# Kernel tuning notes

Hardware: AMD Instinct MI355X
Metric: run time of the kernel (lower is better)

Reference implementation:

```python
import jax, jax.numpy as jnp
import numpy as np

B, H, W = 32, 512, 384
V, F = 6890, 13776


def setup_inputs() -> dict:
    key = jax.random.key(0)
    ks = jax.random.split(key, 8)
    scale = jnp.array([W, H, 1.0], dtype=jnp.float32)
    verts_1 = jax.random.uniform(ks[0], (B, V, 3), dtype=jnp.float32) * scale
    verts_2 = jax.random.uniform(ks[1], (B, V, 3), dtype=jnp.float32) * scale
    # face index per pixel; -1 = background (uint32 0xFFFFFFFF sentinel in original)
    vis_1 = (jax.random.randint(ks[2], (B, H, W), 0, F + 1) - 1).astype(jnp.int32)
    vis_2 = (jax.random.randint(ks[3], (B, H, W), 0, F + 1) - 1).astype(jnp.int32)
    face = jax.random.randint(ks[4], (F, 3), 0, V).astype(jnp.int32)
    vis_sym_mask_1 = (jax.random.uniform(ks[5], (B, H, W)) < 0.5).astype(jnp.float32)
    sym = jax.random.randint(ks[6], (V,), 0, V)
    symmetric_table = jnp.concatenate([sym, jnp.array([-1])]).astype(jnp.int32)
    return {"verts_1": verts_1, "vis_1": vis_1, "verts_2": verts_2, "vis_2": vis_2,
            "face": face, "vis_sym_mask_1": vis_sym_mask_1, "symmetric_table": symmetric_table}


def _pix_grid(h, w):
    # (x, y) pixel coordinates, shape [h, w, 2]
    x = jnp.arange(w, dtype=jnp.float32)
    y = jnp.arange(h, dtype=jnp.float32)
    return jnp.stack(jnp.meshgrid(x, y, indexing="xy"), axis=-1)


def reference(verts_1, vis_1, verts_2, vis_2, face, vis_sym_mask_1, symmetric_table):
    v1 = verts_1[:, :, :2]  # [B,V,2]
    v2 = verts_2[:, :, :2]
    bg = vis_1 < 0
    fc = jnp.where(bg, 0, vis_1)  # safe face id per pixel

    # --- vis_2_onehot: which faces are visible in image 2 ---
    valid2 = vis_2 >= 0
    idx2 = jnp.where(valid2, vis_2, 0)
    bidx = jnp.arange(B)[:, None, None]
    vf2 = jnp.zeros((B, F), jnp.int32).at[bidx, idx2].add(valid2.astype(jnp.int32)) > 0

    # --- cal_corr: barycentric correspondence per pixel ---
    tri = face[fc]  # [B,H,W,3] vertex ids of the face under each pixel
    gather = jax.vmap(lambda verts, t: verts[t])  # per-batch fancy gather
    p1 = gather(v1, tri)  # [B,H,W,3,2] face verts in img1
    p = _pix_grid(H, W)  # [H,W,2]
    a, b_, c = p1[..., 0, :], p1[..., 1, :], p1[..., 2, :]
    e0, e1, e2 = b_ - a, c - a, p - a
    d00 = (e0 * e0).sum(-1); d01 = (e0 * e1).sum(-1); d11 = (e1 * e1).sum(-1)
    d20 = (e2 * e0).sum(-1); d21 = (e2 * e1).sum(-1)
    denom = d00 * d11 - d01 * d01
    denom = jnp.where(jnp.abs(denom) < 1e-12, 1.0, denom)
    wv = (d11 * d20 - d01 * d21) / denom
    ww = (d00 * d21 - d01 * d20) / denom
    bary = jnp.stack([1.0 - wv - ww, wv, ww], axis=-1)  # [B,H,W,3]

    vis2f = vf2[bidx, fc]  # face visible in img2?
    sym_tri = symmetric_table[tri]  # symmetric vertex ids (-1 = none)
    sym_ok = jnp.all(sym_tri >= 0, axis=-1) & (vis_sym_mask_1 > 0)
    use_sym = (~vis2f) & sym_ok & (~bg)
    tri2 = jnp.where(use_sym[..., None], jnp.where(sym_tri >= 0, sym_tri, 0), tri)
    p2 = gather(v2, tri2)  # [B,H,W,3,2] face verts in img2
    corr = jnp.einsum("bhwk,bhwkc->bhwc", bary, p2)  # [B,H,W,2] (u,v)

    has_corr = (~bg) & (vis2f | use_sym)
    corr_mask = jnp.where(bg, 2.0, jnp.where(has_corr, 0.0, 1.0)).astype(jnp.float32)
    corr = jnp.where(has_corr[..., None], corr, 0.0)

    # custom kernel outputs are detached in the original
    corr = jax.lax.stop_gradient(corr)
    corr_mask = jax.lax.stop_gradient(corr_mask)

    # --- pad to square ---
    pad = (H - W) // 2
    corr = corr + jnp.array([pad, 0], dtype=corr.dtype)
    corr = jnp.pad(corr, ((0, 0), (0, 0), (pad, pad), (0, 0)))
    corr_mask = jnp.pad(corr_mask[..., None], ((0, 0), (0, 0), (pad, pad), (0, 0)),
                        constant_values=2.0)  # [B,H,W+2p,1]
    Hp, Wp = H, W + 2 * pad

    # --- corr_to_flow (HWC) then fix_flow: grid = base + (corr - base), normalized ---
    base = _pix_grid(Hp, Wp)  # [Hp,Wp,2]
    flow = corr - base
    grid = base + flow
    gx = 2.0 * grid[..., 0] / max(Wp - 1, 1) - 1.0
    gy = 2.0 * grid[..., 1] / max(Hp - 1, 1) - 1.0
    out_grid = jnp.stack([gx, gy], axis=-1)  # [B,Hp,Wp,2]
    return out_grid, corr_mask
```

## Files before the change

kernel.cpp:

```cpp
#include <hip/hip_runtime.h>

#pragma clang fp contract(off)

#define B_ 32
#define H_ 512
#define W_ 384
#define V_ 6890
#define F_ 13776
#define PAD_ 64
#define WP_ 512
#define NXCD_ 8


__global__ __launch_bounds__(256) void vf2_scatter_kernel(
    const int4* __restrict__ vis_2_v4, unsigned char* __restrict__ vf2)
{
    unsigned bid = blockIdx.x;
    unsigned cpx = gridDim.x >> 3;
    unsigned swz = (bid & 7u) * cpx + (bid >> 3);
    int idx = (int)(swz * blockDim.x + threadIdx.x);
    const int total4 = B_ * H_ * W_ / 4;
    if (idx >= total4) return;
    int4 v = vis_2_v4[idx];
    int b = idx / (H_ * W_ / 4);
    unsigned char* t = vf2 + (size_t)b * F_;
    if (v.x >= 0) t[v.x] = 1;
    if (v.y >= 0) t[v.y] = 1;
    if (v.z >= 0) t[v.z] = 1;
    if (v.w >= 0) t[v.w] = 1;
}

__global__ __launch_bounds__(256) void face_precompute_kernel(
    const float* __restrict__ verts_1,
    const float* __restrict__ verts_2,
    const int*   __restrict__ face,
    const int*   __restrict__ symtab,
    const unsigned char* __restrict__ vf2,
    float4* __restrict__ recs)
{
#pragma clang fp contract(off)
    int idx = blockIdx.x * blockDim.x + threadIdx.x;
    const int total = B_ * F_;
    if (idx >= total) return;
    int f = idx % F_;
    int b = idx / F_;

    int i0 = face[f * 3 + 0];
    int i1 = face[f * 3 + 1];
    int i2 = face[f * 3 + 2];

    const float* v1b = verts_1 + (size_t)b * (V_ * 3);
    float ax = v1b[i0 * 3 + 0], ay = v1b[i0 * 3 + 1];
    float bx = v1b[i1 * 3 + 0], by = v1b[i1 * 3 + 1];
    float cx = v1b[i2 * 3 + 0], cy = v1b[i2 * 3 + 1];

    float e0x = bx - ax, e0y = by - ay;
    float e1x = cx - ax, e1y = cy - ay;

    float d00 = (e0x * e0x) + (e0y * e0y);
    float d01 = (e0x * e1x) + (e0y * e1y);
    float d11 = (e1x * e1x) + (e1y * e1y);

    float denom = (d00 * d11) - (d01 * d01);
    if (fabsf(denom) < 1e-12f) denom = 1.0f;

    bool vis2f = vf2[idx] != 0;

    int s0 = symtab[i0], s1 = symtab[i1], s2 = symtab[i2];
    bool sym_ok = (s0 >= 0) && (s1 >= 0) && (s2 >= 0);

    int t0 = (!vis2f && sym_ok) ? s0 : i0;
    int t1 = (!vis2f && sym_ok) ? s1 : i1;
    int t2 = (!vis2f && sym_ok) ? s2 : i2;

    const float* v2b = verts_2 + (size_t)b * (V_ * 3);
    float q0x = v2b[t0 * 3 + 0], q0y = v2b[t0 * 3 + 1];
    float q1x = v2b[t1 * 3 + 0], q1y = v2b[t1 * 3 + 1];
    float q2x = v2b[t2 * 3 + 0], q2y = v2b[t2 * 3 + 1];

    unsigned u00 = __float_as_uint(d00) | (vis2f  ? 0x80000000u : 0u);
    unsigned u11 = __float_as_uint(d11) | (sym_ok ? 0x80000000u : 0u);

    float4* r = recs + (size_t)idx * 4;
    r[0] = make_float4(ax, ay, e0x, e0y);
    r[1] = make_float4(e1x, e1y, __uint_as_float(u00), d01);
    r[2] = make_float4(__uint_as_float(u11), denom, q0x, q0y);
    r[3] = make_float4(q1x, q1y, q2x, q2y);
}

__global__ __launch_bounds__(256) void flow_main_kernel(
    const int*   __restrict__ vis_1,
    const float* __restrict__ vis_sym_mask_1,
    const float4* __restrict__ recs,
    float* __restrict__ out_grid,
    float* __restrict__ corr_mask)
{
#pragma clang fp contract(off)
    unsigned bid = blockIdx.x;
    unsigned cpx = gridDim.x >> 3;
    unsigned swz = (bid & 7u) * cpx + (bid >> 3);
    int tid  = (int)(swz * blockDim.x + threadIdx.x);
    int base = tid * 2;
    const int total = B_ * H_ * WP_;
    if (base >= total) return;

    int xp  = base % WP_;
    int rem = base / WP_;
    int y   = rem % H_;
    int b   = rem / H_;

    if (xp < PAD_ || xp >= W_ + PAD_) {
        reinterpret_cast<float4*>(out_grid)[base >> 1] =
            make_float4(-1.0f, -1.0f, -1.0f, -1.0f);
        reinterpret_cast<float2*>(corr_mask)[base >> 1] =
            make_float2(2.0f, 2.0f);
        return;
    }

    int x   = xp - PAD_;
    int pin = (b * H_ + y) * W_ + x;

    int2   vv = *reinterpret_cast<const int2*>(vis_1 + pin);
    float2 mm = *reinterpret_cast<const float2*>(vis_sym_mask_1 + pin);

    int   vis[2] = { vv.x, vv.y };
    float msk[2] = { mm.x, mm.y };

    float4 R[2][4];
    bool   bgs[2];
    #pragma unroll
    for (int k = 0; k < 2; ++k) {
        bgs[k] = vis[k] < 0;
        int fc = bgs[k] ? 0 : vis[k];
        const float4* r = recs + ((size_t)b * F_ + fc) * 4;
        R[k][0] = r[0]; R[k][1] = r[1]; R[k][2] = r[2]; R[k][3] = r[3];
    }

    float gxo[2], gyo[2], cmo[2];
    #pragma unroll
    for (int k = 0; k < 2; ++k) {
        float ax = R[k][0].x, ay = R[k][0].y, e0x = R[k][0].z, e0y = R[k][0].w;
        float e1x = R[k][1].x, e1y = R[k][1].y;
        unsigned u00 = __float_as_uint(R[k][1].z);
        float d01 = R[k][1].w;
        unsigned u11 = __float_as_uint(R[k][2].x);
        float denom = R[k][2].y;
        float q0x = R[k][2].z, q0y = R[k][2].w;
        float q1x = R[k][3].x, q1y = R[k][3].y, q2x = R[k][3].z, q2y = R[k][3].w;

        bool vis2f  = (u00 >> 31) != 0;
        bool sym_ok = (u11 >> 31) != 0;
        float d00 = __uint_as_float(u00 & 0x7fffffffu);
        float d11 = __uint_as_float(u11 & 0x7fffffffu);

        float px = (float)(x + k), py = (float)y;
        float e2x = px - ax, e2y = py - ay;

        float d20 = (e2x * e0x) + (e2y * e0y);
        float d21 = (e2x * e1x) + (e2y * e1y);

        float wv = ((d11 * d20) - (d01 * d21)) / denom;
        float ww = ((d00 * d21) - (d01 * d20)) / denom;
        float w0 = (1.0f - wv) - ww;

        bool bg = bgs[k];
        bool use_sym  = (!vis2f) && sym_ok && (msk[k] > 0.0f) && (!bg);
        bool has_corr = (!bg) && (vis2f || use_sym);

        float corr_x = ((w0 * q0x) + (wv * q1x)) + (ww * q2x);
        float corr_y = ((w0 * q0y) + (wv * q1y)) + (ww * q2y);
        if (!has_corr) { corr_x = 0.0f; corr_y = 0.0f; }

        corr_x = corr_x + (float)PAD_;

        float base_x = (float)(xp + k), base_y = (float)y;
        float fx = corr_x - base_x;
        float fy = corr_y - base_y;
        float gxv = base_x + fx;
        float gyv = base_y + fy;

        gxo[k] = ((2.0f * gxv) / (float)(WP_ - 1)) - 1.0f;
        gyo[k] = ((2.0f * gyv) / (float)(H_  - 1)) - 1.0f;
        cmo[k] = bg ? 2.0f : (has_corr ? 0.0f : 1.0f);
    }

    reinterpret_cast<float4*>(out_grid)[base >> 1] =
        make_float4(gxo[0], gyo[0], gxo[1], gyo[1]);
    reinterpret_cast<float2*>(corr_mask)[base >> 1] =
        make_float2(cmo[0], cmo[1]);
}

extern "C" void kernel_launch(void* const* d_in, const int* in_sizes, int n_in,
                              void* d_out, int out_size, void* d_ws, size_t ws_size,
                              hipStream_t stream)
{
    const float* verts_1 = (const float*)d_in[0];
    const int*   vis_1   = (const int*)d_in[1];
    const float* verts_2 = (const float*)d_in[2];
    const int*   vis_2   = (const int*)d_in[3];
    const int*   face    = (const int*)d_in[4];
    const float* vis_sym = (const float*)d_in[5];
    const int*   symtab  = (const int*)d_in[6];

    float* out_grid  = (float*)d_out;
    float* corr_mask = (float*)d_out + (size_t)B_ * H_ * WP_ * 2;

    unsigned char* vf2 = (unsigned char*)d_ws;
    size_t rec_off = ((size_t)B_ * F_ + 63) & ~(size_t)63;
    float4* recs = (float4*)((unsigned char*)d_ws + rec_off);

    hipMemsetAsync(vf2, 0, (size_t)B_ * F_, stream);

    {
        const int total4 = B_ * H_ * W_ / 4;
        const int block  = 256;
        const int grid   = total4 / block;
        vf2_scatter_kernel<<<grid, block, 0, stream>>>(
            (const int4*)vis_2, vf2);
    }
    {
        const int total = B_ * F_;
        const int block = 256;
        face_precompute_kernel<<<(total + block - 1) / block, block, 0, stream>>>(
            verts_1, verts_2, face, symtab, vf2, recs);
    }
    {
        const int total = B_ * H_ * WP_;
        const int block = 256;
        const int grid  = total / (block * 2);
        flow_main_kernel<<<grid, block, 0, stream>>>(
            vis_1, vis_sym, recs, out_grid, corr_mask);
    }
}
```

Measured before the change: 110.6 us.

## Fold barycentric interpolation into per-face affine map and process four pixels per thread

The face precompute kernel now folds the barycentric weights and the image-2 vertex interpolation into a per-face affine map corr = A + B*px + C*py, computed in double precision. This shrinks each face record from 64 to 32 bytes. The main kernel then needs only two FMAs per coordinate instead of dot products and divides. It also handles four pixels per thread with 128-bit loads and stores. The catch is that results can differ slightly from the reference's float operation order, and the precompute kernel now does fp64 math.

```diff
diff --git a/kernel.cpp b/kernel.cpp
--- a/kernel.cpp
+++ b/kernel.cpp
@@ -9,7 +9,6 @@
 #define F_ 13776
 #define PAD_ 64
 #define WP_ 512
-#define NXCD_ 8
 
 
 __global__ __launch_bounds__(256) void vf2_scatter_kernel(
@@ -56,16 +55,13 @@
 
     float e0x = bx - ax, e0y = by - ay;
     float e1x = cx - ax, e1y = cy - ay;
-
     float d00 = (e0x * e0x) + (e0y * e0y);
     float d01 = (e0x * e1x) + (e0y * e1y);
     float d11 = (e1x * e1x) + (e1y * e1y);
-
     float denom = (d00 * d11) - (d01 * d01);
     if (fabsf(denom) < 1e-12f) denom = 1.0f;
 
     bool vis2f = vf2[idx] != 0;
-
     int s0 = symtab[i0], s1 = symtab[i1], s2 = symtab[i2];
     bool sym_ok = (s0 >= 0) && (s1 >= 0) && (s2 >= 0);
 
@@ -78,14 +74,34 @@
     float q1x = v2b[t1 * 3 + 0], q1y = v2b[t1 * 3 + 1];
     float q2x = v2b[t2 * 3 + 0], q2y = v2b[t2 * 3 + 1];
 
-    unsigned u00 = __float_as_uint(d00) | (vis2f  ? 0x80000000u : 0u);
-    unsigned u11 = __float_as_uint(d11) | (sym_ok ? 0x80000000u : 0u);
-
-    float4* r = recs + (size_t)idx * 4;
-    r[0] = make_float4(ax, ay, e0x, e0y);
-    r[1] = make_float4(e1x, e1y, __uint_as_float(u00), d01);
-    r[2] = make_float4(__uint_as_float(u11), denom, q0x, q0y);
-    r[3] = make_float4(q1x, q1y, q2x, q2y);
+    double dd00 = (double)d00, dd01 = (double)d01, dd11 = (double)d11;
+    double dden = (double)denom;
+    double De0x = (double)e0x, De0y = (double)e0y;
+    double De1x = (double)e1x, De1y = (double)e1y;
+
+    double Ux = (dd11 * De0x - dd01 * De1x) / dden;
+    double Uy = (dd11 * De0y - dd01 * De1y) / dden;
+    double Vx = (dd00 * De1x - dd01 * De0x) / dden;
+    double Vy = (dd00 * De1y - dd01 * De0y) / dden;
+
+    double dq1x = (double)q1x - (double)q0x;
+    double dq2x = (double)q2x - (double)q0x;
+    double dq1y = (double)q1y - (double)q0y;
+    double dq2y = (double)q2y - (double)q0y;
+
+    double Bx = Ux * dq1x + Vx * dq2x;
+    double Cx = Uy * dq1x + Vy * dq2x;
+    double By = Ux * dq1y + Vx * dq2y;
+    double Cy = Uy * dq1y + Vy * dq2y;
+
+    double Apx = (double)q0x - (double)ax * Bx - (double)ay * Cx;
+    double Apy = (double)q0y - (double)ax * By - (double)ay * Cy;
+
+    unsigned flags = (vis2f ? 1u : 0u) | (sym_ok ? 2u : 0u);
+
+    float4* r = recs + (size_t)idx * 2;
+    r[0] = make_float4((float)Apx, (float)Bx, (float)Cx, (float)Apy);
+    r[1] = make_float4((float)By, (float)Cy, __uint_as_float(flags), 0.0f);
 }
 
 __global__ __launch_bounds__(256) void flow_main_kernel(
@@ -100,7 +116,7 @@
     unsigned cpx = gridDim.x >> 3;
     unsigned swz = (bid & 7u) * cpx + (bid >> 3);
     int tid  = (int)(swz * blockDim.x + threadIdx.x);
-    int base = tid * 2;
+    int base = tid * 4;
     const int total = B_ * H_ * WP_;
     if (base >= total) return;
 
@@ -109,71 +125,58 @@
     int y   = rem % H_;
     int b   = rem / H_;
 
+    float4* og4 = reinterpret_cast<float4*>(out_grid);
+    float4* cm4 = reinterpret_cast<float4*>(corr_mask);
+
     if (xp < PAD_ || xp >= W_ + PAD_) {
-        reinterpret_cast<float4*>(out_grid)[base >> 1] =
-            make_float4(-1.0f, -1.0f, -1.0f, -1.0f);
-        reinterpret_cast<float2*>(corr_mask)[base >> 1] =
-            make_float2(2.0f, 2.0f);
+        og4[(base >> 1) + 0] = make_float4(-1.0f, -1.0f, -1.0f, -1.0f);
+        og4[(base >> 1) + 1] = make_float4(-1.0f, -1.0f, -1.0f, -1.0f);
+        cm4[base >> 2]       = make_float4(2.0f, 2.0f, 2.0f, 2.0f);
         return;
     }
 
     int x   = xp - PAD_;
     int pin = (b * H_ + y) * W_ + x;
 
-    int2   vv = *reinterpret_cast<const int2*>(vis_1 + pin);
-    float2 mm = *reinterpret_cast<const float2*>(vis_sym_mask_1 + pin);
-
-    int   vis[2] = { vv.x, vv.y };
-    float msk[2] = { mm.x, mm.y };
-
-    float4 R[2][4];
-    bool   bgs[2];
+    int4   vv = *reinterpret_cast<const int4*>(vis_1 + pin);
+    float4 mm = *reinterpret_cast<const float4*>(vis_sym_mask_1 + pin);
+
+    int   vis[4] = { vv.x, vv.y, vv.z, vv.w };
+    float msk[4] = { mm.x, mm.y, mm.z, mm.w };
+
+    float4 R0[4], R1[4];
+    bool   bgs[4];
     #pragma unroll
-    for (int k = 0; k < 2; ++k) {
+    for (int k = 0; k < 4; ++k) {
         bgs[k] = vis[k] < 0;
         int fc = bgs[k] ? 0 : vis[k];
-        const float4* r = recs + ((size_t)b * F_ + fc) * 4;
-        R[k][0] = r[0]; R[k][1] = r[1]; R[k][2] = r[2]; R[k][3] = r[3];
-    }
-
-    float gxo[2], gyo[2], cmo[2];
+        const float4* r = recs + ((size_t)b * F_ + fc) * 2;
+        R0[k] = r[0];
+        R1[k] = r[1];
+    }
+
+    float gxo[4], gyo[4], cmo[4];
     #pragma unroll
-    for (int k = 0; k < 2; ++k) {
-        float ax = R[k][0].x, ay = R[k][0].y, e0x = R[k][0].z, e0y = R[k][0].w;
-        float e1x = R[k][1].x, e1y = R[k][1].y;
-        unsigned u00 = __float_as_uint(R[k][1].z);
-        float d01 = R[k][1].w;
-        unsigned u11 = __float_as_uint(R[k][2].x);
-        float denom = R[k][2].y;
-        float q0x = R[k][2].z, q0y = R[k][2].w;
-        float q1x = R[k][3].x, q1y = R[k][3].y, q2x = R[k][3].z, q2y = R[k][3].w;
-
-        bool vis2f  = (u00 >> 31) != 0;
-        bool sym_ok = (u11 >> 31) != 0;
-        float d00 = __uint_as_float(u00 & 0x7fffffffu);
-        float d11 = __uint_as_float(u11 & 0x7fffffffu);
+    for (int k = 0; k < 4; ++k) {
+        float Apx = R0[k].x, Bx = R0[k].y, Cx = R0[k].z, Apy = R0[k].w;
+        float By  = R1[k].x, Cy = R1[k].y;
+        unsigned flags = __float_as_uint(R1[k].z);
+        bool vis2f  = (flags & 1u) != 0;
+        bool sym_ok = (flags & 2u) != 0;
 
         float px = (float)(x + k), py = (float)y;
-        float e2x = px - ax, e2y = py - ay;
-
-        float d20 = (e2x * e0x) + (e2y * e0y);
-        float d21 = (e2x * e1x) + (e2y * e1y);
-
-        float wv = ((d11 * d20) - (d01 * d21)) / denom;
-        float ww = ((d00 * d21) - (d01 * d20)) / denom;
-        float w0 = (1.0f - wv) - ww;
+
+        float corr_x = ((px * Bx) + (py * Cx)) + Apx;
+        float corr_y = ((px * By) + (py * Cy)) + Apy;
 
         bool bg = bgs[k];
         bool use_sym  = (!vis2f) && sym_ok && (msk[k] > 0.0f) && (!bg);
         bool has_corr = (!bg) && (vis2f || use_sym);
-
-        float corr_x = ((w0 * q0x) + (wv * q1x)) + (ww * q2x);
-        float corr_y = ((w0 * q0y) + (wv * q1y)) + (ww * q2y);
         if (!has_corr) { corr_x = 0.0f; corr_y = 0.0f; }
 
         corr_x = corr_x + (float)PAD_;
 
-        float base_x = (float)(xp + k), base_y = (float)y;
+        float base_x = (float)(xp + k), base_y = py;
         float fx = corr_x - base_x;
         float fy = corr_y - base_y;
         float gxv = base_x + fx;
@@ -184,10 +187,9 @@
         cmo[k] = bg ? 2.0f : (has_corr ? 0.0f : 1.0f);
     }
 
-    reinterpret_cast<float4*>(out_grid)[base >> 1] =
-        make_float4(gxo[0], gyo[0], gxo[1], gyo[1]);
-    reinterpret_cast<float2*>(corr_mask)[base >> 1] =
-        make_float2(cmo[0], cmo[1]);
+    og4[(base >> 1) + 0] = make_float4(gxo[0], gyo[0], gxo[1], gyo[1]);
+    og4[(base >> 1) + 1] = make_float4(gxo[2], gyo[2], gxo[3], gyo[3]);
+    cm4[base >> 2]       = make_float4(cmo[0], cmo[1], cmo[2], cmo[3]);
 }
 
 extern "C" void kernel_launch(void* const* d_in, const int* in_sizes, int n_in,
@@ -227,7 +229,7 @@
     {
         const int total = B_ * H_ * WP_;
         const int block = 256;
-        const int grid  = total / (block * 2);
+        const int grid  = total / (block * 4);
         flow_main_kernel<<<grid, block, 0, stream>>>(
             vis_1, vis_sym, recs, out_grid, corr_mask);
     }
```

Measured after the change: 94.66 us. -14.4%, faster.
